# Performance work log

Hardware: AMD Instinct MI355X
Metric: run time of the kernel (lower is better)

The kernel has to match this reference:

```python
import jax, jax.numpy as jnp
import numpy as np

D_MODEL = 1024
NHEAD = 16
HEAD_DIM = D_MODEL // NHEAD
B, T = 2, 2048


def setup_inputs() -> dict:
    key = jax.random.key(0)
    ks = jax.random.split(key, 11)
    s = 1.0 / np.sqrt(D_MODEL)
    inp = {
        'q': jax.random.normal(ks[0], (B, T, D_MODEL), jnp.float32),
        'k': jax.random.normal(ks[1], (B, T, D_MODEL), jnp.float32),
        'v': jax.random.normal(ks[2], (B, T, D_MODEL), jnp.float32),
        'Wq': jax.random.normal(ks[3], (D_MODEL, D_MODEL), jnp.float32) * s,
        'bq': jnp.zeros((D_MODEL,), jnp.float32),
        'Wk': jax.random.normal(ks[4], (D_MODEL, D_MODEL), jnp.float32) * s,
        'bk': jnp.zeros((D_MODEL,), jnp.float32),
        'Wv': jax.random.normal(ks[5], (D_MODEL, D_MODEL), jnp.float32) * s,
        'bv': jnp.zeros((D_MODEL,), jnp.float32),
        'Wo': jax.random.normal(ks[6], (D_MODEL, D_MODEL), jnp.float32) * s,
        'bo': jnp.zeros((D_MODEL,), jnp.float32),
    }
    return inp


def reference(q, k, v, Wq, bq, Wk, bk, Wv, bv, Wo, bo):
    scale = np.sqrt(HEAD_DIM).astype(np.float32)
    # projections (torch Linear: x @ W.T + b), split heads -> [B, H, T, Dh]
    def proj(x, W, b):
        y = jnp.einsum('btd,ed->bte', x, W) + b
        return y.reshape(B, T, NHEAD, HEAD_DIM).transpose(0, 2, 1, 3)
    qh = proj(q, Wq, bq)
    kh = proj(k, Wk, bk)
    vh = proj(v, Wv, bv)
    scores = jnp.einsum('bhqd,bhkd->bhqk', qh, kh) / scale  # [B,H,T,T]
    weights = jax.nn.softmax(scores, axis=-1)
    out = jnp.einsum('bhqk,bhkd->bhqd', weights, vh)        # [B,H,T,Dh]
    out = out.transpose(0, 2, 1, 3).reshape(B, T, D_MODEL)
    return jnp.einsum('btd,ed->bte', out, Wo) + bo
```

## Files before the change

### kernel.cpp

```cpp
#include <hip/hip_runtime.h>
#include <cstdint>
#include <cstddef>


#define D_MODEL 1024
#define NHEAD   16
#define HDIM    64
#define BATCH   2
#define SEQ     2048
#define BT      (BATCH * SEQ)

#define QSCALE 0.18033688011112043f

typedef __bf16 bf16;
typedef __bf16 bf16x8 __attribute__((ext_vector_type(8)));
typedef __bf16 bf16x4 __attribute__((ext_vector_type(4)));
typedef float  floatx4 __attribute__((ext_vector_type(4)));
typedef short  short4v __attribute__((ext_vector_type(4)));

#define MFMA16(a, b, c) __builtin_amdgcn_mfma_f32_16x16x32_bf16((a), (b), (c), 0, 0, 0)

__device__ __forceinline__ floatx4 MFMA16B(bf16x4 a, bf16x4 b, floatx4 c) {
  return __builtin_amdgcn_mfma_f32_16x16x16bf16_1k(
      __builtin_bit_cast(short4v, a), __builtin_bit_cast(short4v, b), c, 0, 0, 0);
}

__device__ __forceinline__ float fexp2(float x) {
  return __builtin_amdgcn_exp2f(x);
}

__device__ __forceinline__ void async_cp16(const bf16* g, bf16* l) {
  __builtin_amdgcn_global_load_lds(
      (__attribute__((address_space(1))) void*)(g),
      (__attribute__((address_space(3))) void*)(l), 16, 0, 0);
}

__global__ __launch_bounds__(256) void cvt7(
    const float* __restrict__ s0, const float* __restrict__ s1,
    const float* __restrict__ s2, const float* __restrict__ s3,
    const float* __restrict__ s4, const float* __restrict__ s5,
    const float* __restrict__ s6,
    bf16* __restrict__ d0, bf16* __restrict__ d1, bf16* __restrict__ d2,
    bf16* __restrict__ d3, bf16* __restrict__ d4, bf16* __restrict__ d5,
    bf16* __restrict__ d6)
{
  const float* src; bf16* dst; int n4;
  switch (blockIdx.y) {
    case 0:  src = s0; dst = d0; n4 = (BT * D_MODEL) / 4; break;
    case 1:  src = s1; dst = d1; n4 = (BT * D_MODEL) / 4; break;
    case 2:  src = s2; dst = d2; n4 = (BT * D_MODEL) / 4; break;
    case 3:  src = s3; dst = d3; n4 = (D_MODEL * D_MODEL) / 4; break;
    case 4:  src = s4; dst = d4; n4 = (D_MODEL * D_MODEL) / 4; break;
    case 5:  src = s5; dst = d5; n4 = (D_MODEL * D_MODEL) / 4; break;
    default: src = s6; dst = d6; n4 = (D_MODEL * D_MODEL) / 4; break;
  }
  int stride = gridDim.x * blockDim.x;
  for (int i = blockIdx.x * blockDim.x + threadIdx.x; i < n4; i += stride) {
    float4 f = ((const float4*)src)[i];
    bf16x4 h;
    h[0] = (bf16)f.x; h[1] = (bf16)f.y; h[2] = (bf16)f.z; h[3] = (bf16)f.w;
    ((bf16x4*)dst)[i] = h;
  }
}

__device__ __forceinline__ void gemm128_core(
    const bf16* __restrict__ A, const bf16* __restrict__ W,
    int m0, int n0, bf16* As, bf16* Bs, floatx4 acc[4][4])
{
  const int t = threadIdx.x;
  const int l = t & 63, w = t >> 6;
  const int quad = l >> 4, lr = l & 15;
  const int wm = (w >> 1) * 64, wn = (w & 1) * 64;

  floatx4 z = {0.f, 0.f, 0.f, 0.f};
#pragma unroll
  for (int i = 0; i < 4; i++)
#pragma unroll
    for (int j = 0; j < 4; j++) acc[i][j] = z;

  for (int kt = 0; kt < 1024; kt += 32) {
    __syncthreads();
#pragma unroll
    for (int i = 0; i < 2; i++) {
      int c = i * 256 + t;
      int row = c >> 2, ci = c & 3;
      async_cp16(A + (size_t)(m0 + row) * 1024 + kt + ci * 8,
                 As + (i * 256 + w * 64) * 8);
      async_cp16(W + (size_t)(n0 + row) * 1024 + kt + ci * 8,
                 Bs + (i * 256 + w * 64) * 8);
    }
    __syncthreads();

    bf16x8 af[4], bfr[4];
#pragma unroll
    for (int i = 0; i < 4; i++) {
      af[i]  = *(const bf16x8*)(As + (wm + i * 16 + lr) * 32 + quad * 8);
      bfr[i] = *(const bf16x8*)(Bs + (wn + i * 16 + lr) * 32 + quad * 8);
    }
#pragma unroll
    for (int i = 0; i < 4; i++)
#pragma unroll
      for (int j = 0; j < 4; j++)
        acc[i][j] = MFMA16(af[i], bfr[j], acc[i][j]);
  }
}

__global__ __launch_bounds__(256) void qkv_gemm(
    const bf16* __restrict__ qb, const bf16* __restrict__ kb, const bf16* __restrict__ vb,
    const bf16* __restrict__ wq, const bf16* __restrict__ wk, const bf16* __restrict__ wv,
    const float* __restrict__ biasq, const float* __restrict__ biask, const float* __restrict__ biasv,
    bf16* __restrict__ qh, bf16* __restrict__ kh, bf16* __restrict__ vt)
{
  __shared__ bf16 As[128 * 32];
  __shared__ bf16 Bs[128 * 32];
  const int zid = blockIdx.z;
  const bf16* A = (zid == 0) ? qb : ((zid == 1) ? kb : vb);
  const bf16* W = (zid == 0) ? wq : ((zid == 1) ? wk : wv);
  const float* bias = (zid == 0) ? biasq : ((zid == 1) ? biask : biasv);
  const int m0 = blockIdx.x * 128, n0 = blockIdx.y * 128;

  floatx4 acc[4][4];
  gemm128_core(A, W, m0, n0, As, Bs, acc);

  const int t = threadIdx.x, l = t & 63, w = t >> 6;
  const int quad = l >> 4, lr = l & 15;
  const int wm = (w >> 1) * 64, wn = (w & 1) * 64;
  const float sc = (zid == 0) ? QSCALE : 1.0f;

  if (zid < 2) {
    bf16* out = (zid == 0) ? qh : kh;
#pragma unroll
    for (int i = 0; i < 4; i++) {
      int mbase = m0 + wm + i * 16 + quad * 4;
      int b  = mbase >> 11;
      int tq = mbase & 2047;
#pragma unroll
      for (int j = 0; j < 4; j++) {
        int n = n0 + wn + j * 16 + lr;
        float bv = bias[n];
        int h = n >> 6, dh = n & 63;
        bf16* p = out + ((size_t)((b * NHEAD + h) * SEQ + tq)) * HDIM + dh;
#pragma unroll
        for (int r = 0; r < 4; r++)
          p[(size_t)r * HDIM] = (bf16)((acc[i][j][r] + bv) * sc);
      }
    }
  } else {
#pragma unroll
    for (int i = 0; i < 4; i++) {
      int mbase = m0 + wm + i * 16 + quad * 4;
      int b  = mbase >> 11;
      int tq = mbase & 2047;
#pragma unroll
      for (int j = 0; j < 4; j++) {
        int n = n0 + wn + j * 16 + lr;
        float bv = bias[n];
        int h = n >> 6, dh = n & 63;
        bf16x4 pk;
#pragma unroll
        for (int r = 0; r < 4; r++) pk[r] = (bf16)(acc[i][j][r] + bv);
        *(bf16x4*)(vt + ((size_t)((b * NHEAD + h) * HDIM + dh)) * SEQ + tq) = pk;
      }
    }
  }
}

__global__ __launch_bounds__(512, 6) void attn_fused(
    const bf16* __restrict__ qh, const bf16* __restrict__ kh,
    const bf16* __restrict__ vt, bf16* __restrict__ attn)
{
  __shared__ __align__(16) char smem[35840];
  bf16* Ks  = (bf16*)smem;
  bf16* Vts = (bf16*)(smem + 18432);

  const int t = threadIdx.x, l = t & 63, w = t >> 6;
  const int quad = l >> 4, lr = l & 15;
  const int qg = w & 3, half = w >> 2;
  const int bh = blockIdx.y;
  const int qt0 = blockIdx.x * 64;
  const bf16* qg_ = qh + (size_t)bh * SEQ * HDIM;
  const bf16* kg  = kh + (size_t)bh * SEQ * HDIM;
  const bf16* vg  = vt + (size_t)bh * HDIM * SEQ;

  bf16x8 qf[2];
#pragma unroll
  for (int ko = 0; ko < 2; ko++)
    qf[ko] = *(const bf16x8*)(qg_ + (size_t)(qt0 + qg * 16 + lr) * HDIM
                              + ko * 32 + quad * 8);

  floatx4 zz = {0.f, 0.f, 0.f, 0.f};
  floatx4 Oacc[4];
#pragma unroll
  for (int dt = 0; dt < 4; dt++) Oacc[dt] = zz;
  float mrow = -3.0e38f, lrow = 0.f;

  for (int kt0 = 0; kt0 < SEQ; kt0 += 128) {
    __syncthreads();
#pragma unroll
    for (int i = 0; i < 2; i++) {
      int c = t + 512 * i;
      { int row = c >> 3, ci = c & 7;
        *(int4*)(Ks + row * 72 + ci * 8) =
            *(const int4*)(kg + (size_t)(kt0 + row) * HDIM + ci * 8); }
      { int row = c >> 4, ci = c & 15;
        *(int4*)(Vts + row * 136 + ci * 8) =
            *(const int4*)(vg + (size_t)row * SEQ + kt0 + ci * 8); }
    }
    __syncthreads();

    floatx4 s[4];
#pragma unroll
    for (int ni = 0; ni < 4; ni++) {
      const bf16* krow = Ks + (half * 64 + ni * 16 + lr) * 72 + quad * 8;
      bf16x8 k0 = *(const bf16x8*)(krow);
      bf16x8 k1 = *(const bf16x8*)(krow + 32);
      floatx4 a = zz;
      a = MFMA16(k0, qf[0], a);
      a = MFMA16(k1, qf[1], a);
      s[ni] = a;
    }

    float rmax = s[0][0];
#pragma unroll
    for (int ni = 0; ni < 4; ni++)
#pragma unroll
      for (int r = 0; r < 4; r++) rmax = fmaxf(rmax, s[ni][r]);
    rmax = fmaxf(rmax, __shfl_xor(rmax, 16, 64));
    rmax = fmaxf(rmax, __shfl_xor(rmax, 32, 64));
    float mnew = fmaxf(mrow, rmax);
    float al = fexp2(mrow - mnew);
    mrow = mnew;

    bf16x4 pk[4];
    float rsum = 0.f;
#pragma unroll
    for (int ni = 0; ni < 4; ni++)
#pragma unroll
      for (int r = 0; r < 4; r++) {
        float pv = fexp2(s[ni][r] - mnew);
        rsum += pv;
        pk[ni][r] = (bf16)pv;
      }
    rsum += __shfl_xor(rsum, 16, 64);
    rsum += __shfl_xor(rsum, 32, 64);
    lrow = lrow * al + rsum;
#pragma unroll
    for (int dt = 0; dt < 4; dt++)
#pragma unroll
      for (int r = 0; r < 4; r++) Oacc[dt][r] *= al;

#pragma unroll
    for (int ni = 0; ni < 4; ni++)
#pragma unroll
      for (int dt = 0; dt < 4; dt++) {
        bf16x4 vf = *(const bf16x4*)(Vts + (dt * 16 + lr) * 136
                                     + half * 64 + ni * 16 + quad * 4);
        Oacc[dt] = MFMA16B(vf, pk[ni], Oacc[dt]);
      }
  }

  __syncthreads();
  bf16* Ost = (bf16*)(smem + 16896);

  if (half == 1) {
#pragma unroll
    for (int dt = 0; dt < 4; dt++)
      *(floatx4*)(smem + (qg * 4 + dt) * 1024 + l * 16) = Oacc[dt];
    if (quad == 0)
      *(float2*)(smem + 16384 + (qg * 16 + lr) * 8) = make_float2(mrow, lrow);
  }
  __syncthreads();

  if (half == 0) {
    float2 st = *(const float2*)(smem + 16384 + (qg * 16 + lr) * 8);
    float ms = fmaxf(mrow, st.x);
    float fA = fexp2(mrow - ms);
    float fB = fexp2(st.x - ms);
    float inv = 1.0f / (lrow * fA + st.y * fB);
    float gA = fA * inv, gB = fB * inv;
#pragma unroll
    for (int dt = 0; dt < 4; dt++) {
      floatx4 ob = *(const floatx4*)(smem + (qg * 4 + dt) * 1024 + l * 16);
      bf16x4 ov;
#pragma unroll
      for (int r = 0; r < 4; r++)
        ov[r] = (bf16)(Oacc[dt][r] * gA + ob[r] * gB);
      *(bf16x4*)(Ost + (size_t)(qg * 16 + lr) * 72 + dt * 16 + quad * 4) = ov;
    }
  }
  __syncthreads();

  const int b = bh >> 4, h = bh & 15;
  {
    int row = t >> 3, ci = t & 7;
    *(int4*)(attn + ((size_t)b * SEQ + qt0 + row) * D_MODEL + h * HDIM + ci * 8) =
        *(const int4*)(Ost + row * 72 + ci * 8);
  }
}

__global__ __launch_bounds__(256) void oproj_gemm(
    const bf16* __restrict__ attn, const bf16* __restrict__ wo,
    const float* __restrict__ bo, float* __restrict__ out)
{
  __shared__ bf16 As[64 * 32];
  __shared__ bf16 Bs[64 * 32];
  const int m0 = blockIdx.x * 64, n0 = blockIdx.y * 64;
  const int t = threadIdx.x, l = t & 63, w = t >> 6;
  const int quad = l >> 4, lr = l & 15;
  const int wm = (w >> 1) * 32, wn = (w & 1) * 32;

  floatx4 z = {0.f, 0.f, 0.f, 0.f};
  floatx4 acc[2][2];
#pragma unroll
  for (int i = 0; i < 2; i++)
#pragma unroll
    for (int j = 0; j < 2; j++) acc[i][j] = z;

  for (int kt = 0; kt < 1024; kt += 32) {
    __syncthreads();
    {
      int row = t >> 2, ci = t & 3;
      async_cp16(attn + (size_t)(m0 + row) * 1024 + kt + ci * 8,
                 As + (w * 64) * 8);
      async_cp16(wo + (size_t)(n0 + row) * 1024 + kt + ci * 8,
                 Bs + (w * 64) * 8);
    }
    __syncthreads();

    bf16x8 af[2], bfr[2];
#pragma unroll
    for (int i = 0; i < 2; i++) {
      af[i]  = *(const bf16x8*)(As + (wm + i * 16 + lr) * 32 + quad * 8);
      bfr[i] = *(const bf16x8*)(Bs + (wn + i * 16 + lr) * 32 + quad * 8);
    }
#pragma unroll
    for (int i = 0; i < 2; i++)
#pragma unroll
      for (int j = 0; j < 2; j++)
        acc[i][j] = MFMA16(af[i], bfr[j], acc[i][j]);
  }

#pragma unroll
  for (int i = 0; i < 2; i++) {
    int m = m0 + wm + i * 16 + quad * 4;
#pragma unroll
    for (int j = 0; j < 2; j++) {
      int n = n0 + wn + j * 16 + lr;
      float bv = bo[n];
      float* p = out + (size_t)m * D_MODEL + n;
#pragma unroll
      for (int r = 0; r < 4; r++)
        p[(size_t)r * D_MODEL] = acc[i][j][r] + bv;
    }
  }
}

extern "C" void kernel_launch(void* const* d_in, const int* in_sizes, int n_in,
                              void* d_out, int out_size, void* d_ws, size_t ws_size,
                              hipStream_t stream)
{
  const float* q  = (const float*)d_in[0];
  const float* k  = (const float*)d_in[1];
  const float* v  = (const float*)d_in[2];
  const float* Wq = (const float*)d_in[3];
  const float* bq = (const float*)d_in[4];
  const float* Wk = (const float*)d_in[5];
  const float* bk = (const float*)d_in[6];
  const float* Wv = (const float*)d_in[7];
  const float* bv = (const float*)d_in[8];
  const float* Wo = (const float*)d_in[9];
  const float* bo = (const float*)d_in[10];

  const size_t NQ = (size_t)BT * D_MODEL;
  const size_t NW = (size_t)D_MODEL * D_MODEL;

  bf16* p = (bf16*)d_ws;
  bf16* qb   = p; p += NQ;
  bf16* kb   = p; p += NQ;
  bf16* vb   = p; p += NQ;
  bf16* wqb  = p; p += NW;
  bf16* wkb  = p; p += NW;
  bf16* wvb  = p; p += NW;
  bf16* wob  = p; p += NW;
  bf16* qhp  = p; p += NQ;
  bf16* khp  = p; p += NQ;
  bf16* vtp  = p; p += NQ;
  bf16* attn = p; p += NQ;

  cvt7<<<dim3(1024, 7, 1), 256, 0, stream>>>(q, k, v, Wq, Wk, Wv, Wo,
                                             qb, kb, vb, wqb, wkb, wvb, wob);
  qkv_gemm<<<dim3(32, 8, 3), 256, 0, stream>>>(qb, kb, vb, wqb, wkb, wvb,
                                               bq, bk, bv, qhp, khp, vtp);
  attn_fused<<<dim3(32, 32, 1), 512, 0, stream>>>(qhp, khp, vtp, attn);
  oproj_gemm<<<dim3(64, 16, 1), 256, 0, stream>>>(attn, wob, bo, (float*)d_out);
}
```

Before: 258.4 us.

## Double-buffer K/V tiles with async copies and 128-query attention blocks

Reworks the fused attention kernel so each block handles 128 queries with every wave owning 16 query rows over the full 128-key tile. The split-key half reduction and its merge step are removed. K and V tiles are now double-buffered in 64KB of shared memory and loaded with async global-to-LDS copies, prefetching the next tile during compute. An XOR swizzle replaces the padded LDS layout to avoid bank conflicts. This halves the grid and lowers target occupancy from 6 to 4, trading parallelism for fewer redundant K/V loads and overlap of loads with compute.

```diff
diff --git a/kernel.cpp b/kernel.cpp
--- a/kernel.cpp
+++ b/kernel.cpp
@@ -165,27 +165,37 @@
   }
 }
 
-__global__ __launch_bounds__(512, 6) void attn_fused(
+__global__ __launch_bounds__(512, 4) void attn_fused(
     const bf16* __restrict__ qh, const bf16* __restrict__ kh,
     const bf16* __restrict__ vt, bf16* __restrict__ attn)
 {
-  __shared__ __align__(16) char smem[35840];
-  bf16* Ks  = (bf16*)smem;
-  bf16* Vts = (bf16*)(smem + 18432);
+  __shared__ __align__(16) char smem[65536];
 
   const int t = threadIdx.x, l = t & 63, w = t >> 6;
   const int quad = l >> 4, lr = l & 15;
-  const int qg = w & 3, half = w >> 2;
   const int bh = blockIdx.y;
-  const int qt0 = blockIdx.x * 64;
-  const bf16* qg_ = qh + (size_t)bh * SEQ * HDIM;
-  const bf16* kg  = kh + (size_t)bh * SEQ * HDIM;
-  const bf16* vg  = vt + (size_t)bh * HDIM * SEQ;
+  const int qt0 = blockIdx.x * 128;
+  const bf16* qg = qh + (size_t)bh * SEQ * HDIM;
+  const bf16* kg = kh + (size_t)bh * SEQ * HDIM;
+  const bf16* vg = vt + (size_t)bh * HDIM * SEQ;
+
+  int krow0 = (w * 2) * 8 + (l >> 3);
+  int krow1 = (w * 2 + 1) * 8 + (l >> 3);
+  int kcl0  = (l & 7) ^ (krow0 & 7);
+  int kcl1  = (l & 7) ^ (krow1 & 7);
+  int vrow0 = (w * 2) * 4 + (l >> 4);
+  int vrow1 = (w * 2 + 1) * 4 + (l >> 4);
+  int vcl0  = (l & 15) ^ (vrow0 & 15);
+  int vcl1  = (l & 15) ^ (vrow1 & 15);
+  const bf16* kga = kg + (size_t)krow0 * HDIM + kcl0 * 8;
+  const bf16* kgb = kg + (size_t)krow1 * HDIM + kcl1 * 8;
+  const bf16* vga = vg + (size_t)vrow0 * SEQ + vcl0 * 8;
+  const bf16* vgb = vg + (size_t)vrow1 * SEQ + vcl1 * 8;
 
   bf16x8 qf[2];
 #pragma unroll
   for (int ko = 0; ko < 2; ko++)
-    qf[ko] = *(const bf16x8*)(qg_ + (size_t)(qt0 + qg * 16 + lr) * HDIM
+    qf[ko] = *(const bf16x8*)(qg + (size_t)(qt0 + w * 16 + lr) * HDIM
                               + ko * 32 + quad * 8);
 
   floatx4 zz = {0.f, 0.f, 0.f, 0.f};
@@ -194,26 +204,36 @@
   for (int dt = 0; dt < 4; dt++) Oacc[dt] = zz;
   float mrow = -3.0e38f, lrow = 0.f;
 
-  for (int kt0 = 0; kt0 < SEQ; kt0 += 128) {
-    __syncthreads();
-#pragma unroll
-    for (int i = 0; i < 2; i++) {
-      int c = t + 512 * i;
-      { int row = c >> 3, ci = c & 7;
-        *(int4*)(Ks + row * 72 + ci * 8) =
-            *(const int4*)(kg + (size_t)(kt0 + row) * HDIM + ci * 8); }
-      { int row = c >> 4, ci = c & 15;
-        *(int4*)(Vts + row * 136 + ci * 8) =
-            *(const int4*)(vg + (size_t)row * SEQ + kt0 + ci * 8); }
-    }
-    __syncthreads();
-
-    floatx4 s[4];
-#pragma unroll
-    for (int ni = 0; ni < 4; ni++) {
-      const bf16* krow = Ks + (half * 64 + ni * 16 + lr) * 72 + quad * 8;
-      bf16x8 k0 = *(const bf16x8*)(krow);
-      bf16x8 k1 = *(const bf16x8*)(krow + 32);
+  {
+    bf16* Kb = (bf16*)smem;
+    bf16* Vb = (bf16*)(smem + 16384);
+    async_cp16(kga, Kb + (w * 2) * 512);
+    async_cp16(kgb, Kb + (w * 2 + 1) * 512);
+    async_cp16(vga, Vb + (w * 2) * 512);
+    async_cp16(vgb, Vb + (w * 2 + 1) * 512);
+  }
+
+  for (int kt = 0; kt < 16; kt++) {
+    const int p = kt & 1;
+    __syncthreads();
+    if (kt + 1 < 16) {
+      bf16* Kb = (bf16*)(smem + (1 - p) * 32768);
+      bf16* Vb = (bf16*)(smem + (1 - p) * 32768 + 16384);
+      int off = (kt + 1) * 128;
+      async_cp16(kga + (size_t)off * HDIM, Kb + (w * 2) * 512);
+      async_cp16(kgb + (size_t)off * HDIM, Kb + (w * 2 + 1) * 512);
+      async_cp16(vga + off, Vb + (w * 2) * 512);
+      async_cp16(vgb + off, Vb + (w * 2 + 1) * 512);
+    }
+    const bf16* Ks  = (const bf16*)(smem + p * 32768);
+    const bf16* Vts = (const bf16*)(smem + p * 32768 + 16384);
+
+    floatx4 s[8];
+#pragma unroll
+    for (int ni = 0; ni < 8; ni++) {
+      const bf16* krow = Ks + (ni * 16 + lr) * 64;
+      bf16x8 k0 = *(const bf16x8*)(krow + ((quad ^ (lr & 7)) * 8));
+      bf16x8 k1 = *(const bf16x8*)(krow + (((quad + 4) ^ (lr & 7)) * 8));
       floatx4 a = zz;
       a = MFMA16(k0, qf[0], a);
       a = MFMA16(k1, qf[1], a);
@@ -222,7 +242,7 @@
 
     float rmax = s[0][0];
 #pragma unroll
-    for (int ni = 0; ni < 4; ni++)
+    for (int ni = 0; ni < 8; ni++)
 #pragma unroll
       for (int r = 0; r < 4; r++) rmax = fmaxf(rmax, s[ni][r]);
     rmax = fmaxf(rmax, __shfl_xor(rmax, 16, 64));
@@ -231,10 +251,10 @@
     float al = fexp2(mrow - mnew);
     mrow = mnew;
 
-    bf16x4 pk[4];
+    bf16x4 pk[8];
     float rsum = 0.f;
 #pragma unroll
-    for (int ni = 0; ni < 4; ni++)
+    for (int ni = 0; ni < 8; ni++)
 #pragma unroll
       for (int r = 0; r < 4; r++) {
         float pv = fexp2(s[ni][r] - mnew);
@@ -250,49 +270,32 @@
       for (int r = 0; r < 4; r++) Oacc[dt][r] *= al;
 
 #pragma unroll
-    for (int ni = 0; ni < 4; ni++)
+    for (int ni = 0; ni < 8; ni++)
 #pragma unroll
       for (int dt = 0; dt < 4; dt++) {
-        bf16x4 vf = *(const bf16x4*)(Vts + (dt * 16 + lr) * 136
-                                     + half * 64 + ni * 16 + quad * 4);
+        bf16x4 vf = *(const bf16x4*)(Vts + (dt * 16 + lr) * 128
+                                     + (((ni * 2 + (quad >> 1)) ^ lr) * 8)
+                                     + (quad & 1) * 4);
         Oacc[dt] = MFMA16B(vf, pk[ni], Oacc[dt]);
       }
   }
 
+  float inv = 1.0f / lrow;
+  bf16* Ost = (bf16*)smem;
+#pragma unroll
+  for (int dt = 0; dt < 4; dt++) {
+    bf16x4 ov;
+#pragma unroll
+    for (int r = 0; r < 4; r++) ov[r] = (bf16)(Oacc[dt][r] * inv);
+    *(bf16x4*)(Ost + (size_t)(w * 16 + lr) * 72 + dt * 16 + quad * 4) = ov;
+  }
   __syncthreads();
-  bf16* Ost = (bf16*)(smem + 16896);
-
-  if (half == 1) {
-#pragma unroll
-    for (int dt = 0; dt < 4; dt++)
-      *(floatx4*)(smem + (qg * 4 + dt) * 1024 + l * 16) = Oacc[dt];
-    if (quad == 0)
-      *(float2*)(smem + 16384 + (qg * 16 + lr) * 8) = make_float2(mrow, lrow);
-  }
-  __syncthreads();
-
-  if (half == 0) {
-    float2 st = *(const float2*)(smem + 16384 + (qg * 16 + lr) * 8);
-    float ms = fmaxf(mrow, st.x);
-    float fA = fexp2(mrow - ms);
-    float fB = fexp2(st.x - ms);
-    float inv = 1.0f / (lrow * fA + st.y * fB);
-    float gA = fA * inv, gB = fB * inv;
-#pragma unroll
-    for (int dt = 0; dt < 4; dt++) {
-      floatx4 ob = *(const floatx4*)(smem + (qg * 4 + dt) * 1024 + l * 16);
-      bf16x4 ov;
-#pragma unroll
-      for (int r = 0; r < 4; r++)
-        ov[r] = (bf16)(Oacc[dt][r] * gA + ob[r] * gB);
-      *(bf16x4*)(Ost + (size_t)(qg * 16 + lr) * 72 + dt * 16 + quad * 4) = ov;
-    }
-  }
-  __syncthreads();
 
   const int b = bh >> 4, h = bh & 15;
-  {
-    int row = t >> 3, ci = t & 7;
+#pragma unroll
+  for (int i = 0; i < 2; i++) {
+    int c = t + 512 * i;
+    int row = c >> 3, ci = c & 7;
     *(int4*)(attn + ((size_t)b * SEQ + qt0 + row) * D_MODEL + h * HDIM + ci * 8) =
         *(const int4*)(Ost + row * 72 + ci * 8);
   }
@@ -391,6 +394,6 @@
                                              qb, kb, vb, wqb, wkb, wvb, wob);
   qkv_gemm<<<dim3(32, 8, 3), 256, 0, stream>>>(qb, kb, vb, wqb, wkb, wvb,
                                                bq, bk, bv, qhp, khp, vtp);
-  attn_fused<<<dim3(32, 32, 1), 512, 0, stream>>>(qhp, khp, vtp, attn);
+  attn_fused<<<dim3(16, 32, 1), 512, 0, stream>>>(qhp, khp, vtp, attn);
   oproj_gemm<<<dim3(64, 16, 1), 256, 0, stream>>>(attn, wob, bo, (float*)d_out);
 }
```

Measured after the change: 226.5 us. -12.3%, faster.
